# Kernel optimization log

Measured on AMD Instinct MI355X. Metric: run time of the kernel, lower is better.

The kernel has to match this reference:

```python
import jax, jax.numpy as jnp
import numpy as np
from math import sqrt

EMA_W = 0.3  # ema_weight
LN_EPS = 1e-5


def setup_inputs() -> dict:
    key = jax.random.key(0)
    ks = jax.random.split(key, 16)
    B, L, H, E = 8, 1024, 8, 64
    d_ff, dp_rank = 2048, 8
    inp = {
        "queries": jax.random.normal(ks[0], (B, L, H, E), jnp.float32),
        "keys": jax.random.normal(ks[1], (B, L, H, E), jnp.float32),
        "values": jax.random.normal(ks[2], (B, L, H, E), jnp.float32),
        "attn_mask": jnp.zeros((B, 1, L, L), jnp.bool_),
        # dynamic-projection mlp: Linear(E, dp_rank)
        "mlp_w": jax.random.normal(ks[3], (E, dp_rank), jnp.float32) / sqrt(E),
        "mlp_b": jnp.zeros((dp_rank,), jnp.float32),
        # ff_1: Linear(E,d_ff) -> GELU -> Linear(d_ff,E)
        "ff1_w1": jax.random.normal(ks[4], (E, d_ff), jnp.float32) / sqrt(E),
        "ff1_b1": jnp.zeros((d_ff,), jnp.float32),
        "ff1_w2": jax.random.normal(ks[5], (d_ff, E), jnp.float32) / sqrt(d_ff),
        "ff1_b2": jnp.zeros((E,), jnp.float32),
        # ff_2
        "ff2_w1": jax.random.normal(ks[6], (E, d_ff), jnp.float32) / sqrt(E),
        "ff2_b1": jnp.zeros((d_ff,), jnp.float32),
        "ff2_w2": jax.random.normal(ks[7], (d_ff, E), jnp.float32) / sqrt(d_ff),
        "ff2_b2": jnp.zeros((E,), jnp.float32),
        # LayerNorm(E)
        "ln_w": jnp.ones((E,), jnp.float32),
        "ln_b": jnp.zeros((E,), jnp.float32),
    }
    return inp


def _dynamic_projection(src, mlp_w, mlp_b):
    # src: [B,L,H,E] -> softmax over dp_rank, then einsum 'blhe,blhr->blhe'
    sm = jax.nn.softmax(src @ mlp_w + mlp_b, axis=-1)  # [B,L,H,R]
    return jnp.einsum('blhe,blhr->blhe', src, sm)


def _ffn(x, w1, b1, w2, b2):
    return jax.nn.gelu(x @ w1 + b1, approximate=False) @ w2 + b2


def reference(queries, keys, values, attn_mask,
              mlp_w, mlp_b,
              ff1_w1, ff1_b1, ff1_w2, ff1_b2,
              ff2_w1, ff2_b1, ff2_w2, ff2_b2,
              ln_w, ln_b):
    E = queries.shape[-1]
    scale = 1.0 / sqrt(24.0)   # hardcoded in source
    scale1 = 1.0 / sqrt(E)

    dp_values = _dynamic_projection(values, mlp_w, mlp_b)
    dp_keys = _dynamic_projection(keys, mlp_w, mlp_b)

    # ema state starts at zeros every forward, so ema = (1-w) * x
    ema_queries = (1.0 - EMA_W) * queries
    ema_keys = (1.0 - EMA_W) * dp_keys

    # NOTE: source masks a scores tensor that is then overwritten; mask has
    # no effect on the output, so attn_mask is unused (kept for fidelity).
    scores = jnp.einsum('blhe,bshe->bhls', ema_queries, ema_keys)
    scores1 = jnp.einsum('blhe,bshe->bhls', queries, keys)

    A = jax.nn.softmax(scale * scores, axis=-1)    # dropout = identity (eval)
    A1 = jax.nn.softmax(scale1 * scores1, axis=-1)

    V = jnp.einsum('bhls,bshd->blhd', A, dp_values)
    V1 = jnp.einsum('bhls,bshd->blhd', A1, values)

    src = _ffn(V, ff1_w1, ff1_b1, ff1_w2, ff1_b2) + _ffn(V1, ff2_w1, ff2_b1, ff2_w2, ff2_b2)

    mu = jnp.mean(src, axis=-1, keepdims=True)
    var = jnp.mean(jnp.square(src - mu), axis=-1, keepdims=True)
    out = (src - mu) * jax.lax.rsqrt(var + LN_EPS) * ln_w + ln_b
    return out
```

## Files before the change

kernel.cpp:

```cpp
#include <hip/hip_runtime.h>

typedef _Float16 f16x8 __attribute__((ext_vector_type(8)));
typedef _Float16 f16x2 __attribute__((ext_vector_type(2)));
typedef float f32x4 __attribute__((ext_vector_type(4)));
typedef float f32x16 __attribute__((ext_vector_type(16)));
typedef unsigned short u16x8 __attribute__((ext_vector_type(8)));
typedef unsigned int u32x4 __attribute__((ext_vector_type(4)));

static __device__ __forceinline__ unsigned short f2h(float x) {
  return __builtin_bit_cast(unsigned short, (_Float16)x);
}
static __device__ __forceinline__ float h2f(unsigned short u) {
  return (float)__builtin_bit_cast(_Float16, u);
}

static __device__ __forceinline__ f16x2 gelu_pk(f16x2 x) {
  const f16x2 P4 = {(_Float16)4.0f, (_Float16)4.0f};
  const f16x2 N4 = {(_Float16)-4.0f, (_Float16)-4.0f};
  const f16x2 C1 = {(_Float16)0.392761f, (_Float16)0.392761f};
  const f16x2 C3 = {(_Float16)-0.0512736f, (_Float16)-0.0512736f};
  const f16x2 C5 = {(_Float16)0.00376322f, (_Float16)0.00376322f};
  const f16x2 C7 = {(_Float16)-0.000100287f, (_Float16)-0.000100287f};
  const f16x2 HF = {(_Float16)0.5f, (_Float16)0.5f};
  const f16x2 ONE = {(_Float16)1.0f, (_Float16)1.0f};
  const f16x2 ZRO = {(_Float16)0.0f, (_Float16)0.0f};
  f16x2 xc = __builtin_elementwise_max(__builtin_elementwise_min(x, P4), N4);
  f16x2 u = xc * xc;
  f16x2 p = __builtin_elementwise_fma(
      __builtin_elementwise_fma(__builtin_elementwise_fma(C7, u, C5), u, C3),
      u, C1);
  f16x2 q = __builtin_elementwise_fma(xc, p, HF);
  f16x2 qc = __builtin_elementwise_max(__builtin_elementwise_min(q, ONE), ZRO);
  return x * qc;
}

static __device__ __forceinline__ int sig16(int v) {
  return (v & ~12) | ((v & 4) << 1) | ((v & 8) >> 1);
}

__global__ __launch_bounds__(256) void k_prep(
    const float* __restrict__ vsrc, const float* __restrict__ ksrc,
    const float* __restrict__ w11, const float* __restrict__ w21,
    const float* __restrict__ w12, const float* __restrict__ w22,
    unsigned short* __restrict__ vtb, unsigned short* __restrict__ kf16,
    unsigned short* __restrict__ w1t1, unsigned short* __restrict__ w2t1,
    unsigned short* __restrict__ w1t2, unsigned short* __restrict__ w2t2) {
  int bid = blockIdx.x, tid = threadIdx.x;
  if (bid >= 1152) {
    int kb = bid - 1152, bh = kb >> 4, lt = kb & 15, b = bh >> 3, h = bh & 7;
    const float* src = ksrc + (((b * 1024 + lt * 64) * 8 + h) << 6);
    unsigned short* dst = kf16 + bh * 65536 + lt * 64 * 64;
#pragma unroll
    for (int i = 0; i < 2; ++i) {
      int c = tid + i * 256, r = c >> 3, c0 = (c & 7) * 8;
      const float* s = src + r * 512 + c0;
      f32x4 a = *(const f32x4*)s, b4 = *(const f32x4*)(s + 4);
      u16x8 vv;
#pragma unroll
      for (int j = 0; j < 4; ++j) { vv[j] = f2h(a[j]); vv[j + 4] = f2h(b4[j]); }
      *(u16x8*)(dst + r * 64 + c0) = vv;
    }
    return;
  }
  __shared__ unsigned short t[64][72];
  const float* src; unsigned short* dst; int srs, drs;
  bool isw2 = false;
  if (bid < 1024) {
    int bh = bid >> 4, lt = bid & 15, b = bh >> 3, h = bh & 7;
    src = vsrc + (((b * 1024 + lt * 64) * 8 + h) << 6); srs = 512;
    dst = vtb + bh * 65536 + lt * 64; drs = 1024;
  } else {
    int wb = bid - 1024, which = wb >> 5, ti = wb & 31;
    isw2 = (which & 1);
    if (which == 0)      { src = w11 + ti * 64;   srs = 2048; dst = w1t1 + ti * 4096; drs = 64; }
    else if (which == 1) { src = w21 + ti * 4096; srs = 64;   dst = w2t1 + ti * 64;   drs = 2048; }
    else if (which == 2) { src = w12 + ti * 64;   srs = 2048; dst = w1t2 + ti * 4096; drs = 64; }
    else                 { src = w22 + ti * 4096; srs = 64;   dst = w2t2 + ti * 64;   drs = 2048; }
  }
#pragma unroll
  for (int i = 0; i < 2; ++i) {
    int c = tid + i * 256, r = c >> 3, c0 = (c & 7) * 8;
    const float* s = src + r * srs + c0;
    int tr = isw2 ? sig16(r) : r;
#pragma unroll
    for (int j = 0; j < 8; ++j) t[c0 + j][tr] = f2h(s[j]);
  }
  __syncthreads();
#pragma unroll
  for (int i = 0; i < 2; ++i) {
    int c = tid + i * 256, r = c >> 3, c0 = (c & 7) * 8;
    u16x8 vv;
#pragma unroll
    for (int j = 0; j < 8; ++j) vv[j] = t[r][c0 + j];
    *(u16x8*)(dst + r * drs + c0) = vv;
  }
}

__global__ __launch_bounds__(64) __attribute__((amdgpu_waves_per_eu(2, 4)))
void k_attn(
    const float* __restrict__ q, const unsigned short* __restrict__ kf16,
    const unsigned short* __restrict__ vtb,
    unsigned short* __restrict__ Vo, unsigned short* __restrict__ V1o) {
  int bid = blockIdx.x;
  int swz = (bid & 7) * 512 + (bid >> 3);
  int bh = swz >> 6, rem = swz & 63, qt = rem >> 2, w = rem & 3;
  int b = bh >> 3, h = bh & 7;
  int lane = threadIdx.x & 63, t = lane & 15, g = lane >> 4;

  __shared__ unsigned short Pl[2][1024];

  f16x8 aq[2];
  {
    int row = qt * 64 + w * 16 + t;
    const float* qp = q + ((b * 1024 + row) * 8 + h) * 64;
#pragma unroll
    for (int ks = 0; ks < 2; ++ks) {
      f32x4 q0 = *(const f32x4*)(qp + ks * 32 + g * 8);
      f32x4 q1 = *(const f32x4*)(qp + ks * 32 + g * 8 + 4);
      f16x8 a;
#pragma unroll
      for (int j = 0; j < 4; ++j) { a[j] = (_Float16)q0[j]; a[j + 4] = (_Float16)q1[j]; }
      aq[ks] = a;
    }
  }

  const float scl[2] = {0.14429954f, 0.18033688f};
  float lsp[2][4];
  f32x4 o[2][4];
#pragma unroll
  for (int i = 0; i < 4; ++i) {
    lsp[0][i] = 0.f; lsp[1][i] = 0.f;
    o[0][i] = (f32x4){0, 0, 0, 0}; o[1][i] = (f32x4){0, 0, 0, 0};
  }

  const unsigned short* kfb = kf16 + bh * 65536;
  const unsigned short* vbase = vtb + bh * 65536;

  f16x8 bk[8];
#pragma unroll
  for (int ks = 0; ks < 2; ++ks)
#pragma unroll
    for (int nt = 0; nt < 4; ++nt)
      bk[ks * 4 + nt] = *(const f16x8*)(kfb + (nt * 16 + t) * 64 + (ks * 4 + g) * 8);

#pragma unroll 1
  for (int kt = 0; kt < 16; ++kt) {
    f16x8 bv[8];
#pragma unroll
    for (int ks = 0; ks < 2; ++ks)
#pragma unroll
      for (int nt = 0; nt < 4; ++nt)
        bv[ks * 4 + nt] = *(const f16x8*)(vbase + (nt * 16 + t) * 1024 + kt * 64 + (ks * 4 + g) * 8);

    f32x4 s[4];
#pragma unroll
    for (int nt = 0; nt < 4; ++nt) s[nt] = (f32x4){0, 0, 0, 0};
#pragma unroll
    for (int ks = 0; ks < 2; ++ks)
#pragma unroll
      for (int nt = 0; nt < 4; ++nt)
        s[nt] = __builtin_amdgcn_mfma_f32_16x16x32_f16(aq[ks], bk[ks * 4 + nt], s[nt], 0, 0, 0);

    if (kt < 15) {
#pragma unroll
      for (int ks = 0; ks < 2; ++ks)
#pragma unroll
        for (int nt = 0; nt < 4; ++nt)
          bk[ks * 4 + nt] = *(const f16x8*)(kfb + ((kt + 1) * 64 + nt * 16 + t) * 64 + (ks * 4 + g) * 8);
    }
    __builtin_amdgcn_sched_barrier(0);

#pragma unroll
    for (int v = 0; v < 2; ++v) {
      float pr[4][4];
#pragma unroll
      for (int nt = 0; nt < 4; ++nt)
#pragma unroll
        for (int reg = 0; reg < 4; ++reg)
          pr[nt][reg] = fminf(exp2f(s[nt][reg] * scl[v]), 60000.0f);
#pragma unroll
      for (int nt = 0; nt < 4; ++nt)
#pragma unroll
        for (int reg = 0; reg < 4; ++reg) {
          int r = g * 4 + reg, sc = nt * 16 + t;
          Pl[v][r * 64 + ((((sc >> 3) ^ (r & 7)) << 3) | (sc & 7))] = f2h(pr[nt][reg]);
        }
#pragma unroll
      for (int reg = 0; reg < 4; ++reg)
        lsp[v][reg] += (pr[0][reg] + pr[1][reg]) + (pr[2][reg] + pr[3][reg]);
    }
    asm volatile("s_waitcnt lgkmcnt(0)" ::: "memory");
#pragma unroll
    for (int v = 0; v < 2; ++v)
#pragma unroll
      for (int ks = 0; ks < 2; ++ks) {
        f16x8 ap = *(const f16x8*)&Pl[v][t * 64 + (((ks * 4 + g) ^ (t & 7)) << 3)];
#pragma unroll
        for (int nt = 0; nt < 4; ++nt)
          o[v][nt] = __builtin_amdgcn_mfma_f32_16x16x32_f16(ap, bv[ks * 4 + nt], o[v][nt], 0, 0, 0);
      }
  }

#pragma unroll
  for (int v = 0; v < 2; ++v)
#pragma unroll
    for (int dd = 1; dd < 16; dd <<= 1)
#pragma unroll
      for (int reg = 0; reg < 4; ++reg)
        lsp[v][reg] += __shfl_xor(lsp[v][reg], dd);

#pragma unroll
  for (int nt = 0; nt < 4; ++nt)
#pragma unroll
    for (int reg = 0; reg < 4; ++reg) {
      int row = qt * 64 + w * 16 + g * 4 + reg;
      int idx = ((b * 1024 + row) * 8 + h) * 64 + nt * 16 + t;
      float r0 = __builtin_amdgcn_rcpf(lsp[0][reg]);
      float r1 = __builtin_amdgcn_rcpf(lsp[1][reg]);
      Vo[idx]  = f2h(o[0][nt][reg] * r0);
      V1o[idx] = f2h(o[1][nt][reg] * r1);
    }
}

static __device__ __forceinline__ void compute_chunk(
    int j, const unsigned short* __restrict__ W1buf,
    const unsigned short* __restrict__ W2buf,
    const float* __restrict__ biasL, const f16x8 (&bx)[4],
    f32x16& acc0, f32x16& acc1, int t5, int hh) {
  f32x16 d0, d1;
#pragma unroll
  for (int rq = 0; rq < 4; ++rq) {
    f32x4 bb0 = *(const f32x4*)(biasL + j * 64 + rq * 8 + hh * 4);
    f32x4 bb1 = *(const f32x4*)(biasL + j * 64 + 32 + rq * 8 + hh * 4);
#pragma unroll
    for (int jj = 0; jj < 4; ++jj) { d0[rq * 4 + jj] = bb0[jj]; d1[rq * 4 + jj] = bb1[jj]; }
  }
#pragma unroll
  for (int ks = 0; ks < 4; ++ks) {
    int fr0 = t5;
    f16x8 aw0 = *(const f16x8*)&W1buf[fr0 * 64 + (((ks * 2 + hh) ^ (fr0 & 7)) << 3)];
    d0 = __builtin_amdgcn_mfma_f32_32x32x16_f16(aw0, bx[ks], d0, 0, 0, 0);
    int fr1 = 32 + t5;
    f16x8 aw1 = *(const f16x8*)&W1buf[fr1 * 64 + (((ks * 2 + hh) ^ (fr1 & 7)) << 3)];
    d1 = __builtin_amdgcn_mfma_f32_32x32x16_f16(aw1, bx[ks], d1, 0, 0, 0);
  }
#pragma unroll
  for (int g = 0; g < 4; ++g) {
    u32x4 av;
#pragma unroll
    for (int q = 0; q < 4; ++q) {
      int base = (g & 1) * 8 + 2 * q;
      float lo = (g < 2) ? d0[base] : d1[base];
      float hi = (g < 2) ? d0[base + 1] : d1[base + 1];
      f16x2 hx = __builtin_bit_cast(f16x2, __builtin_amdgcn_cvt_pkrtz(lo, hi));
      av[q] = __builtin_bit_cast(unsigned, gelu_pk(hx));
    }
    f16x8 hb = __builtin_bit_cast(f16x8, av);
    int er0 = t5;
    f16x8 wa0 = *(const f16x8*)&W2buf[er0 * 64 + (((g * 2 + hh) ^ (er0 & 7)) << 3)];
    acc0 = __builtin_amdgcn_mfma_f32_32x32x16_f16(wa0, hb, acc0, 0, 0, 0);
    int er1 = 32 + t5;
    f16x8 wa1 = *(const f16x8*)&W2buf[er1 * 64 + (((g * 2 + hh) ^ (er1 & 7)) << 3)];
    acc1 = __builtin_amdgcn_mfma_f32_32x32x16_f16(wa1, hb, acc1, 0, 0, 0);
  }
}

__global__ __launch_bounds__(256) void k_ffn(
    const unsigned short* __restrict__ Vo, const unsigned short* __restrict__ V1o,
    const unsigned short* __restrict__ w1ta, const unsigned short* __restrict__ w2ta,
    const unsigned short* __restrict__ w1tb, const unsigned short* __restrict__ w2tb,
    const float* __restrict__ b1a, const float* __restrict__ b1b,
    unsigned short* __restrict__ p0, unsigned short* __restrict__ p1,
    unsigned short* __restrict__ p2, unsigned short* __restrict__ p3) {
  int bid = blockIdx.x;
  int quar = bid >> 9, rb = bid & 511;
  int tid = threadIdx.x, w = tid >> 6, lane = tid & 63;
  int t5 = lane & 31, hh = lane >> 5;
  int rowbase = rb * 128 + w * 32;
  unsigned short* pout = (quar == 0) ? p0 : (quar == 1) ? p1 : (quar == 2) ? p2 : p3;

  __shared__ unsigned short W1c[4096];
  __shared__ unsigned short W2c[4096];
  __shared__ float biasL[2][512];

  if (tid < 128) {
    *(f32x4*)&biasL[0][tid * 4] = *(const f32x4*)(b1a + quar * 512 + tid * 4);
    *(f32x4*)&biasL[1][tid * 4] = *(const f32x4*)(b1b + quar * 512 + tid * 4);
  }

  f32x16 acc0, acc1;
#pragma unroll
  for (int i = 0; i < 16; ++i) { acc0[i] = 0.f; acc1[i] = 0.f; }

  int r0 = tid >> 3, c8 = tid & 7;
  int sw = (c8 ^ (r0 & 7)) << 3;

#pragma unroll 1
  for (int ffn = 0; ffn < 2; ++ffn) {
    const unsigned short* X = ffn ? V1o : Vo;
    const unsigned short* w1t = ffn ? w1tb : w1ta;
    const unsigned short* w2t = ffn ? w2tb : w2ta;
    f16x8 bx[4];
#pragma unroll
    for (int ks = 0; ks < 4; ++ks)
      bx[ks] = *(const f16x8*)(X + (rowbase + t5) * 64 + ks * 16 + hh * 8);

    int cbase = quar * 8;
    u16x8 ra0 = *(const u16x8*)(w1t + (cbase * 64 + r0) * 64 + c8 * 8);
    u16x8 ra1 = *(const u16x8*)(w1t + (cbase * 64 + r0 + 32) * 64 + c8 * 8);
    u16x8 rb0 = *(const u16x8*)(w2t + r0 * 2048 + cbase * 64 + c8 * 8);
    u16x8 rb1 = *(const u16x8*)(w2t + (r0 + 32) * 2048 + cbase * 64 + c8 * 8);

#pragma unroll 1
    for (int j = 0; j < 8; ++j) {
      __syncthreads();
      *(u16x8*)&W1c[r0 * 64 + sw] = ra0;
      *(u16x8*)&W2c[r0 * 64 + sw] = rb0;
      *(u16x8*)&W1c[(r0 + 32) * 64 + sw] = ra1;
      *(u16x8*)&W2c[(r0 + 32) * 64 + sw] = rb1;
      __syncthreads();
      if (j < 7) {
        int c1 = cbase + j + 1;
        ra0 = *(const u16x8*)(w1t + (c1 * 64 + r0) * 64 + c8 * 8);
        ra1 = *(const u16x8*)(w1t + (c1 * 64 + r0 + 32) * 64 + c8 * 8);
        rb0 = *(const u16x8*)(w2t + r0 * 2048 + c1 * 64 + c8 * 8);
        rb1 = *(const u16x8*)(w2t + (r0 + 32) * 2048 + c1 * 64 + c8 * 8);
      }
      compute_chunk(j, W1c, W2c, &biasL[ffn][0], bx, acc0, acc1, t5, hh);
    }
  }

  int orow = rowbase + t5;
#pragma unroll
  for (int q = 0; q < 8; ++q) {
    int e0 = (2 * q & 3) + 8 * (q >> 1) + 4 * hh;
    unsigned pa = __builtin_bit_cast(unsigned,
        __builtin_amdgcn_cvt_pkrtz(acc0[2 * q], acc0[2 * q + 1]));
    unsigned pb = __builtin_bit_cast(unsigned,
        __builtin_amdgcn_cvt_pkrtz(acc1[2 * q], acc1[2 * q + 1]));
    *(unsigned*)(pout + orow * 64 + e0) = pa;
    *(unsigned*)(pout + orow * 64 + 32 + e0) = pb;
  }
}

__global__ __launch_bounds__(256) void k_reduce(
    const unsigned short* __restrict__ p0, const unsigned short* __restrict__ p1,
    const unsigned short* __restrict__ p2, const unsigned short* __restrict__ p3,
    const float* __restrict__ b2a, const float* __restrict__ b2b,
    const float* __restrict__ lnw, const float* __restrict__ lnb,
    float* __restrict__ out) {
  int tid = threadIdx.x, w = tid >> 6, lane = tid & 63;
  float bias = b2a[lane] + b2b[lane];
  float lw = lnw[lane], lb = lnb[lane];
  int wid = blockIdx.x * 4 + w;
#pragma unroll 4
  for (int i = 0; i < 16; ++i) {
    int r = wid * 16 + i;
    int ix = r * 64 + lane;
    float v = (h2f(p0[ix]) + h2f(p1[ix])) + (h2f(p2[ix]) + h2f(p3[ix])) + bias;
    float s1 = v, s2 = v * v;
#pragma unroll
    for (int dd = 1; dd < 64; dd <<= 1) {
      s1 += __shfl_xor(s1, dd);
      s2 += __shfl_xor(s2, dd);
    }
    float mu = s1 * 0.015625f;
    float var = s2 * 0.015625f - mu * mu;
    out[ix] = (v - mu) * rsqrtf(var + 1e-5f) * lw + lb;
  }
}

extern "C" void kernel_launch(void* const* d_in, const int* in_sizes, int n_in,
                              void* d_out, int out_size, void* d_ws, size_t ws_size,
                              hipStream_t stream) {
  (void)in_sizes; (void)n_in; (void)out_size; (void)ws_size;
  const float* q   = (const float*)d_in[0];
  const float* k   = (const float*)d_in[1];
  const float* v   = (const float*)d_in[2];
  const float* w11 = (const float*)d_in[6];
  const float* b11 = (const float*)d_in[7];
  const float* w21 = (const float*)d_in[8];
  const float* b21 = (const float*)d_in[9];
  const float* w12 = (const float*)d_in[10];
  const float* b12 = (const float*)d_in[11];
  const float* w22 = (const float*)d_in[12];
  const float* b22 = (const float*)d_in[13];
  const float* lnw = (const float*)d_in[14];
  const float* lnb = (const float*)d_in[15];

  unsigned short* vtb  = (unsigned short*)d_ws;
  unsigned short* Vo   = vtb + 4194304;
  unsigned short* V1o  = Vo + 4194304;
  unsigned short* w1t1 = V1o + 4194304;
  unsigned short* w2t1 = w1t1 + 131072;
  unsigned short* w1t2 = w2t1 + 131072;
  unsigned short* w2t2 = w1t2 + 131072;
  unsigned short* part1 = w2t2 + 131072;
  unsigned short* kf16  = part1 + 4194304;
  unsigned short* part3 = kf16 + 4194304;
  unsigned short* part0 = vtb;
  unsigned short* part2 = kf16;

  k_prep<<<dim3(2176), dim3(256), 0, stream>>>(v, k, w11, w21, w12, w22,
                                               vtb, kf16, w1t1, w2t1, w1t2, w2t2);
  k_attn<<<dim3(4096), dim3(64), 0, stream>>>(q, kf16, vtb, Vo, V1o);
  k_ffn<<<dim3(2048), dim3(256), 0, stream>>>(Vo, V1o, w1t1, w2t1, w1t2, w2t2,
                                              b11, b12, part0, part1, part2, part3);
  k_reduce<<<dim3(1024), dim3(256), 0, stream>>>(part0, part1, part2, part3,
                                                 b21, b22, lnw, lnb, (float*)d_out);
}
```

Baseline: 247.3 us.

## Software-pipeline attention loop: overlap previous tile's PV MFMA with current exp

Restructures the key-tile loop so the P·V MFMAs for tile kt-1 run while tile kt's exponentials are computed. P is double-buffered in shared memory and V loads lag by one tile, with an epilogue handling the last tile. The waves_per_eu attribute and the explicit sched_barrier and lgkmcnt wait are removed, giving the compiler more freedom. This doubles LDS use and may raise register pressure. With only one wave per block, the missing wait between the LDS writes and the next iteration's reads relies on the compiler inserting it correctly.

```diff
diff --git a/kernel.cpp b/kernel.cpp
--- a/kernel.cpp
+++ b/kernel.cpp
@@ -96,8 +96,7 @@
   }
 }
 
-__global__ __launch_bounds__(64) __attribute__((amdgpu_waves_per_eu(2, 4)))
-void k_attn(
+__global__ __launch_bounds__(64) void k_attn(
     const float* __restrict__ q, const unsigned short* __restrict__ kf16,
     const unsigned short* __restrict__ vtb,
     unsigned short* __restrict__ Vo, unsigned short* __restrict__ V1o) {
@@ -107,7 +106,7 @@
   int b = bh >> 3, h = bh & 7;
   int lane = threadIdx.x & 63, t = lane & 15, g = lane >> 4;
 
-  __shared__ unsigned short Pl[2][1024];
+  __shared__ unsigned short Pl[2][2][1024];
 
   f16x8 aq[2];
   {
@@ -146,11 +145,13 @@
 #pragma unroll 1
   for (int kt = 0; kt < 16; ++kt) {
     f16x8 bv[8];
-#pragma unroll
-    for (int ks = 0; ks < 2; ++ks)
-#pragma unroll
-      for (int nt = 0; nt < 4; ++nt)
-        bv[ks * 4 + nt] = *(const f16x8*)(vbase + (nt * 16 + t) * 1024 + kt * 64 + (ks * 4 + g) * 8);
+    if (kt > 0) {
+#pragma unroll
+      for (int ks = 0; ks < 2; ++ks)
+#pragma unroll
+        for (int nt = 0; nt < 4; ++nt)
+          bv[ks * 4 + nt] = *(const f16x8*)(vbase + (nt * 16 + t) * 1024 + (kt - 1) * 64 + (ks * 4 + g) * 8);
+    }
 
     f32x4 s[4];
 #pragma unroll
@@ -168,33 +169,57 @@
         for (int nt = 0; nt < 4; ++nt)
           bk[ks * 4 + nt] = *(const f16x8*)(kfb + ((kt + 1) * 64 + nt * 16 + t) * 64 + (ks * 4 + g) * 8);
     }
-    __builtin_amdgcn_sched_barrier(0);
-
+
+    float pr[2][4][4];
 #pragma unroll
     for (int v = 0; v < 2; ++v) {
-      float pr[4][4];
 #pragma unroll
       for (int nt = 0; nt < 4; ++nt)
 #pragma unroll
         for (int reg = 0; reg < 4; ++reg)
-          pr[nt][reg] = fminf(exp2f(s[nt][reg] * scl[v]), 60000.0f);
+          pr[v][nt][reg] = fminf(exp2f(s[nt][reg] * scl[v]), 60000.0f);
+#pragma unroll
+      for (int reg = 0; reg < 4; ++reg)
+        lsp[v][reg] += (pr[v][0][reg] + pr[v][1][reg]) + (pr[v][2][reg] + pr[v][3][reg]);
+    }
+
+    if (kt > 0) {
+      int pp = (kt - 1) & 1;
+#pragma unroll
+      for (int v = 0; v < 2; ++v)
+#pragma unroll
+        for (int ks = 0; ks < 2; ++ks) {
+          f16x8 ap = *(const f16x8*)&Pl[pp][v][t * 64 + (((ks * 4 + g) ^ (t & 7)) << 3)];
+#pragma unroll
+          for (int nt = 0; nt < 4; ++nt)
+            o[v][nt] = __builtin_amdgcn_mfma_f32_16x16x32_f16(ap, bv[ks * 4 + nt], o[v][nt], 0, 0, 0);
+        }
+    }
+
+#pragma unroll
+    for (int v = 0; v < 2; ++v)
 #pragma unroll
       for (int nt = 0; nt < 4; ++nt)
 #pragma unroll
         for (int reg = 0; reg < 4; ++reg) {
           int r = g * 4 + reg, sc = nt * 16 + t;
-          Pl[v][r * 64 + ((((sc >> 3) ^ (r & 7)) << 3) | (sc & 7))] = f2h(pr[nt][reg]);
+          Pl[kt & 1][v][r * 64 + ((((sc >> 3) ^ (r & 7)) << 3) | (sc & 7))] =
+              f2h(pr[v][nt][reg]);
         }
-#pragma unroll
-      for (int reg = 0; reg < 4; ++reg)
-        lsp[v][reg] += (pr[0][reg] + pr[1][reg]) + (pr[2][reg] + pr[3][reg]);
-    }
-    asm volatile("s_waitcnt lgkmcnt(0)" ::: "memory");
+  }
+
+  {
+    f16x8 bv[8];
+#pragma unroll
+    for (int ks = 0; ks < 2; ++ks)
+#pragma unroll
+      for (int nt = 0; nt < 4; ++nt)
+        bv[ks * 4 + nt] = *(const f16x8*)(vbase + (nt * 16 + t) * 1024 + 15 * 64 + (ks * 4 + g) * 8);
 #pragma unroll
     for (int v = 0; v < 2; ++v)
 #pragma unroll
       for (int ks = 0; ks < 2; ++ks) {
-        f16x8 ap = *(const f16x8*)&Pl[v][t * 64 + (((ks * 4 + g) ^ (t & 7)) << 3)];
+        f16x8 ap = *(const f16x8*)&Pl[1][v][t * 64 + (((ks * 4 + g) ^ (t & 7)) << 3)];
 #pragma unroll
         for (int nt = 0; nt < 4; ++nt)
           o[v][nt] = __builtin_amdgcn_mfma_f32_16x16x32_f16(ap, bv[ks * 4 + nt], o[v][nt], 0, 0, 0);
```

Measured after the change: 248.1 us. Within noise of the previous version (+0.3%).
